# Optimization experiments

Hardware: AMD Instinct MI355X
Metric: run time of the kernel (lower is better)

## Reference

```python
import jax, jax.numpy as jnp
import numpy as np

B, N_O, N_Q = 2, 512, 512
POS_DIM, LATENT, HEADS, HEAD_DIM, OUT_DIM = 3, 256, 8, 32, 128
HD = HEADS * HEAD_DIM  # == LATENT here


def _lin(key, fan_in, fan_out):
    return jax.random.normal(key, (fan_in, fan_out), jnp.float32) / np.sqrt(fan_in)


def setup_inputs() -> dict:
    key = jax.random.key(0)
    ks = jax.random.split(key, 12)
    return {
        'h_obs': jax.random.normal(ks[0], (B, N_O, LATENT), jnp.float32),
        'pos_obs': jax.random.uniform(ks[1], (B, N_O, POS_DIM), jnp.float32),
        'pos_query': jax.random.uniform(ks[2], (B, N_Q, POS_DIM), jnp.float32),
        'fw1': _lin(ks[3], LATENT, LATENT), 'fb1': jnp.zeros((LATENT,), jnp.float32),
        'fw2': _lin(ks[4], LATENT, HD), 'fb2': jnp.zeros((HD,), jnp.float32),
        'log_sigma': jnp.zeros((HEADS,), jnp.float32),
        'kw1': _lin(ks[5], POS_DIM * 3, LATENT), 'kb1': jnp.zeros((LATENT,), jnp.float32),
        'kw2': _lin(ks[6], LATENT, HEADS), 'kb2': jnp.zeros((HEADS,), jnp.float32),
        'ow': _lin(ks[7], HD, OUT_DIM), 'ob': jnp.zeros((OUT_DIM,), jnp.float32),
        'vw': _lin(ks[8], HD, OUT_DIM), 'vb': jnp.zeros((OUT_DIM,), jnp.float32),
    }


def reference(h_obs, pos_obs, pos_query, fw1, fb1, fw2, fb2, log_sigma,
              kw1, kb1, kw2, kb2, ow, ob, vw, vb):
    Bv, No, _ = h_obs.shape
    Nq = pos_query.shape[1]
    # feature net -> values [B, H, N_o, D]
    v = jax.nn.relu(h_obs @ fw1 + fb1) @ fw2 + fb2
    v = v.reshape(Bv, No, HEADS, HEAD_DIM).transpose(0, 2, 1, 3)
    # pairwise relative positions [B, Nq, No, P]
    pos_q = pos_query[:, :, None, :]
    pos_o = pos_obs[:, None, :, :]
    rel = pos_q - pos_o
    dist2 = jnp.sum(rel ** 2, axis=-1)  # [B, Nq, No]
    sigma = jnp.exp(log_sigma)[None, :, None, None]
    rbf = jnp.exp(-dist2[:, None] / (sigma ** 2 + 1e-6))  # [B, H, Nq, No]
    # kernel MLP on concatenated pairwise positions [B, Nq, No, 3P] -> [B, H, Nq, No]
    ki = jnp.concatenate([
        jnp.broadcast_to(pos_q, (Bv, Nq, No, POS_DIM)),
        jnp.broadcast_to(pos_o, (Bv, Nq, No, POS_DIM)),
        rel], axis=-1)
    delta = (jax.nn.relu(ki @ kw1 + kb1) @ kw2 + kb2).transpose(0, 3, 1, 2)
    logits = jnp.log(rbf + 1e-8) + delta
    weights = jax.nn.softmax(logits, axis=-1)  # [B, H, Nq, No]
    # weighted mean over observations
    v_mean = jnp.einsum('bhqo,bhod->bhqd', weights, v)  # [B, H, Nq, D]
    h_query = v_mean.transpose(0, 2, 1, 3).reshape(Bv, Nq, HD)
    # weighted variance: sum_o w * (v_o - v_mean)^2
    residual = v[:, :, None, :, :] - v_mean[:, :, :, None, :]  # [B, H, Nq, No, D]
    var = jnp.sum(weights[..., None] * residual ** 2, axis=3)  # [B, H, Nq, D]
    var = var.transpose(0, 2, 1, 3).reshape(Bv, Nq, HD)
    mean = h_query @ ow + ob
    var_out = jax.nn.softplus(var @ vw + vb)
    return (mean, var_out)
```

## Files before the change

### kernel.cpp

```cpp
#include <hip/hip_runtime.h>
#include <math.h>

#define NB 2
#define NO 512
#define NQ 512
#define OUT_DIM 128
#define LPAD 516

typedef __attribute__((ext_vector_type(8))) _Float16 half8;
typedef __attribute__((ext_vector_type(4))) _Float16 half4;
typedef __attribute__((ext_vector_type(4))) float f32x4;

__device__ __forceinline__ float softplus_f(float x) {
  return x > 0.0f ? x + log1pf(expf(-x)) : log1pf(expf(x));
}
__device__ __forceinline__ half8 splat8(_Float16 v) {
  return (half8){v, v, v, v, v, v, v, v};
}
__device__ __forceinline__ half8 fma8(half8 a, half8 b, half8 c) {
  return __builtin_elementwise_fma(a, b, c);
}
__device__ __forceinline__ half8 max8(half8 a, half8 b) {
  return __builtin_elementwise_max(a, b);
}
__device__ __forceinline__ void gll16(const void* g, void* l) {
  __builtin_amdgcn_global_load_lds(
      (const __attribute__((address_space(1))) unsigned int*)g,
      (__attribute__((address_space(3))) unsigned int*)l, 16, 0, 0);
}

__global__ __launch_bounds__(1024) void prep_kernel(
    const float* __restrict__ h_obs, const float* __restrict__ fw1,
    const float* __restrict__ fb1, const float* __restrict__ fw2,
    const float* __restrict__ fb2, _Float16* __restrict__ VT)
{
  __shared__ float s_red[4][4][256];
  __shared__ float s_hid[4][256];
  const int n  = threadIdx.x & 255;
  const int ks = threadIdx.x >> 8;
  const int r0 = blockIdx.x * 4;
  const int k0 = ks * 64;
  float a0 = 0.f, a1 = 0.f, a2 = 0.f, a3 = 0.f;
  #pragma unroll 8
  for (int kk = 0; kk < 64; ++kk) {
    int k = k0 + kk;
    float w = fw1[k * 256 + n];
    a0 = fmaf(h_obs[(r0 + 0) * 256 + k], w, a0);
    a1 = fmaf(h_obs[(r0 + 1) * 256 + k], w, a1);
    a2 = fmaf(h_obs[(r0 + 2) * 256 + k], w, a2);
    a3 = fmaf(h_obs[(r0 + 3) * 256 + k], w, a3);
  }
  s_red[ks][0][n] = a0; s_red[ks][1][n] = a1;
  s_red[ks][2][n] = a2; s_red[ks][3][n] = a3;
  __syncthreads();
  if (ks == 0) {
    float bb = fb1[n];
    #pragma unroll
    for (int r = 0; r < 4; ++r) {
      float v = s_red[0][r][n] + s_red[1][r][n] + s_red[2][r][n] + s_red[3][r][n] + bb;
      s_hid[r][n] = fmaxf(v, 0.f);
    }
  }
  __syncthreads();
  float c0 = 0.f, c1 = 0.f, c2 = 0.f, c3 = 0.f;
  #pragma unroll 8
  for (int kk = 0; kk < 64; ++kk) {
    int k = k0 + kk;
    float w = fw2[k * 256 + n];
    c0 = fmaf(s_hid[0][k], w, c0);
    c1 = fmaf(s_hid[1][k], w, c1);
    c2 = fmaf(s_hid[2][k], w, c2);
    c3 = fmaf(s_hid[3][k], w, c3);
  }
  __syncthreads();
  s_red[ks][0][n] = c0; s_red[ks][1][n] = c1;
  s_red[ks][2][n] = c2; s_red[ks][3][n] = c3;
  __syncthreads();
  if (ks == 0) {
    float bb = fb2[n];
    float vr[4];
    #pragma unroll
    for (int r = 0; r < 4; ++r)
      vr[r] = s_red[0][r][n] + s_red[1][r][n] + s_red[2][r][n] + s_red[3][r][n] + bb;
    const int h  = n >> 5, d = n & 31;
    const int bb_ = r0 >> 9, o0 = r0 & 511;
    half4 pv;
    #pragma unroll
    for (int r = 0; r < 4; ++r) pv[r] = (_Float16)vr[r];
    *(half4*)(VT + ((size_t)((bb_ * 8 + h) * 32 + d)) * 512 + o0) = pv;
  }
}

__global__ __launch_bounds__(512, 4) void attn_fused(
    const _Float16* __restrict__ VT,
    const float* __restrict__ kw1,
    const float* __restrict__ kb1,
    const float* __restrict__ kw2,
    const float* __restrict__ kb2,
    const float* __restrict__ log_sigma,
    const float* __restrict__ pos_obs,
    const float* __restrict__ pos_query,
    float* __restrict__ HVg)
{
  __shared__ __align__(16) float s_logits[2][8 * LPAD];
  __shared__ __align__(16) _Float16 s_P16[2][8][520];
  __shared__ half8 s_Bh[512];
  __shared__ __align__(16) float s_pool[256];
  __shared__ __align__(16) float s_po[3][516];
  __shared__ __align__(16) _Float16 s_co[3][264];

  _Float16* s_aq2 = (_Float16*)s_pool;

  const int t   = threadIdx.x;
  const int bq0 = blockIdx.x * 2;
  const int b   = bq0 >> 9;

  float pqx[2], pqy[2], pqz[2];
  #pragma unroll
  for (int q = 0; q < 2; ++q) {
    pqx[q] = pos_query[(bq0 + q) * 3 + 0];
    pqy[q] = pos_query[(bq0 + q) * 3 + 1];
    pqz[q] = pos_query[(bq0 + q) * 3 + 2];
  }
  {
    const int q = t >> 8, j = t & 255;
    float c0 = kw1[0 * 256 + j] + kw1[6 * 256 + j];
    float c1 = kw1[1 * 256 + j] + kw1[7 * 256 + j];
    float c2 = kw1[2 * 256 + j] + kw1[8 * 256 + j];
    s_aq2[q * 256 + j] = (_Float16)
        fmaf(pqx[q], c0, fmaf(pqy[q], c1, fmaf(pqz[q], c2, kb1[j])));
  }
  if (t < 256) {
    const int j = t;
    s_co[0][j] = (_Float16)(kw1[3 * 256 + j] - kw1[6 * 256 + j]);
    s_co[1][j] = (_Float16)(kw1[4 * 256 + j] - kw1[7 * 256 + j]);
    s_co[2][j] = (_Float16)(kw1[5 * 256 + j] - kw1[8 * 256 + j]);
  }
  {
    const int o = t;
    const float* p = pos_obs + (size_t)(b * NO + o) * 3;
    float px = p[0], py = p[1], pz = p[2];
    s_po[0][o] = px; s_po[1][o] = py; s_po[2][o] = pz;
    float d2q[2];
    #pragma unroll
    for (int q = 0; q < 2; ++q) {
      float r0 = pqx[q] - px, r1 = pqy[q] - py, r2 = pqz[q] - pz;
      d2q[q] = r0 * r0 + r1 * r1 + r2 * r2;
    }
    #pragma unroll
    for (int h = 0; h < 8; ++h) {
      float sg  = __expf(log_sigma[h]);
      float inv = 1.0f / (sg * sg + 1e-6f);
      float kbv = kb2[h];
      s_logits[0][h * LPAD + o] = fmaxf(-d2q[0] * inv, -18.420681f) + kbv;
      s_logits[1][h * LPAD + o] = fmaxf(-d2q[1] * inv, -18.420681f) + kbv;
    }
  }
  {
    const int kstep = t >> 6, lane = t & 63;
    const int nh = lane & 15;
    const int kb_ = kstep * 32 + ((lane >> 4) & 3) * 8;
    half8 b8;
    #pragma unroll
    for (int i = 0; i < 8; ++i) {
      float v = (nh < 8) ? kw2[(kb_ + i) * 8 + nh] : 0.f;
      b8[i] = (_Float16)v;
    }
    s_Bh[kstep * 64 + lane] = b8;
  }
  __syncthreads();

  {
    const int wave = t >> 6, lane = t & 63;
    const int quad = lane >> 4, mrow = lane & 15;
    const int tb   = wave * 4;
    _Float16 pxh[4], pyh[4], pzh[4];
    #pragma unroll
    for (int jt = 0; jt < 4; ++jt) {
      const int o = (tb + jt) * 16 + mrow;
      pxh[jt] = (_Float16)s_po[0][o];
      pyh[jt] = (_Float16)s_po[1][o];
      pzh[jt] = (_Float16)s_po[2][o];
    }
    f32x4 C[2][4];
    #pragma unroll
    for (int q = 0; q < 2; ++q)
      #pragma unroll
      for (int jt = 0; jt < 4; ++jt) C[q][jt] = (f32x4){0.f, 0.f, 0.f, 0.f};

    const half8 z8 = {0, 0, 0, 0, 0, 0, 0, 0};
    #pragma unroll
    for (int kstep = 0; kstep < 8; ++kstep) {
      const int koff = kstep * 32 + quad * 8;
      half8 c0 = *(const half8*)&s_co[0][koff];
      half8 c1 = *(const half8*)&s_co[1][koff];
      half8 c2 = *(const half8*)&s_co[2][koff];
      half8 aq0 = *(const half8*)(s_aq2 + koff);
      half8 aq1 = *(const half8*)(s_aq2 + 256 + koff);
      half8 bh  = s_Bh[kstep * 64 + lane];
      #pragma unroll
      for (int jt = 0; jt < 4; ++jt) {
        half8 ao = fma8(splat8(pxh[jt]), c0,
                   fma8(splat8(pyh[jt]), c1, splat8(pzh[jt]) * c2));
        half8 a0 = max8(aq0 + ao, z8);
        half8 a1 = max8(aq1 + ao, z8);
        C[0][jt] = __builtin_amdgcn_mfma_f32_16x16x32_f16(a0, bh, C[0][jt], 0, 0, 0);
        C[1][jt] = __builtin_amdgcn_mfma_f32_16x16x32_f16(a1, bh, C[1][jt], 0, 0, 0);
      }
    }
    const int hh = lane & 15;
    if (hh < 8) {
      #pragma unroll
      for (int q = 0; q < 2; ++q)
        #pragma unroll
        for (int jt = 0; jt < 4; ++jt) {
          const int ob2 = (tb + jt) * 16 + quad * 4;
          #pragma unroll
          for (int r = 0; r < 4; ++r)
            s_logits[q][hh * LPAD + ob2 + r] += C[q][jt][r];
        }
    }
  }
  __syncthreads();

  {
    const int h = t >> 6, lane = t & 63;
    const int kg = lane >> 4, dl = lane & 15;
    char* stg0 = (char*)s_Bh + h * 1024;
    char* b1   = (char*)&s_logits[0][h * LPAD];
    char* b3   = b1 + 1024;
    char* b2   = (char*)&s_logits[1][h * LPAD];
    const _Float16* vsrc = VT + ((size_t)(b * 8 + h) << 14)
                         + (lane >> 1) * 512 + (lane & 1) * 8;
    gll16(vsrc, stg0);

    float invq0, invq1;
    {
      const float* pl0 = &s_logits[0][h * LPAD];
      const float* pl1 = &s_logits[1][h * LPAD];
      float l0[8], l1[8];
      float m0 = -1e30f, m1 = -1e30f;
      #pragma unroll
      for (int k = 0; k < 8; ++k) {
        l0[k] = pl0[k * 64 + lane];
        l1[k] = pl1[k * 64 + lane];
        m0 = fmaxf(m0, l0[k]);
        m1 = fmaxf(m1, l1[k]);
      }
      #pragma unroll
      for (int off = 32; off >= 1; off >>= 1) {
        m0 = fmaxf(m0, __shfl_xor(m0, off, 64));
        m1 = fmaxf(m1, __shfl_xor(m1, off, 64));
      }
      float s0 = 0.f, s1 = 0.f;
      _Float16* pp0 = &s_P16[0][h][0];
      _Float16* pp1 = &s_P16[1][h][0];
      #pragma unroll
      for (int k = 0; k < 8; ++k) {
        float p0 = __expf(l0[k] - m0);
        float p1 = __expf(l1[k] - m1);
        s0 += p0; s1 += p1;
        pp0[k * 64 + lane] = (_Float16)p0;
        pp1[k * 64 + lane] = (_Float16)p1;
      }
      #pragma unroll
      for (int off = 32; off >= 1; off >>= 1) {
        s0 += __shfl_xor(s0, off, 64);
        s1 += __shfl_xor(s1, off, 64);
      }
      invq0 = 1.0f / s0; invq1 = 1.0f / s1;
    }
    gll16(vsrc + 16, b1);
    gll16(vsrc + 32, b2);
    gll16(vsrc + 48, b3);

    const char* pE = ((kg & 2) ? b1 : stg0) + dl * 32 + (kg & 1) * 16;
    const char* pO = ((kg & 2) ? b3 : b2)   + dl * 32 + (kg & 1) * 16;
    const _Float16* pB = &s_P16[lane & 1][h][0];
    f32x4 Cm0 = {0.f, 0.f, 0.f, 0.f}, Cm1 = Cm0, Cv0 = Cm0, Cv1 = Cm0;
    #pragma unroll
    for (int kp = 0; kp < 8; ++kp) {
      asm volatile("s_waitcnt vmcnt(2)" ::: "memory");
      {
        half8 am0 = *(const half8*)(pE);
        half8 am1 = *(const half8*)(pE + 512);
        half8 pb  = *(const half8*)(pB + (2 * kp) * 32 + kg * 8);
        half8 av0 = am0 * am0;
        half8 av1 = am1 * am1;
        __builtin_amdgcn_s_setprio(1);
        Cm0 = __builtin_amdgcn_mfma_f32_16x16x32_f16(am0, pb, Cm0, 0, 0, 0);
        Cm1 = __builtin_amdgcn_mfma_f32_16x16x32_f16(am1, pb, Cm1, 0, 0, 0);
        Cv0 = __builtin_amdgcn_mfma_f32_16x16x32_f16(av0, pb, Cv0, 0, 0, 0);
        Cv1 = __builtin_amdgcn_mfma_f32_16x16x32_f16(av1, pb, Cv1, 0, 0, 0);
        __builtin_amdgcn_s_setprio(0);
      }
      if (kp < 7) {
        asm volatile("s_waitcnt lgkmcnt(0)" ::: "memory");
        gll16(vsrc + (4 * kp + 4) * 16, stg0);
        gll16(vsrc + (4 * kp + 5) * 16, b1);
      }
      if (kp < 7) asm volatile("s_waitcnt vmcnt(2)" ::: "memory");
      else        asm volatile("s_waitcnt vmcnt(0)" ::: "memory");
      {
        half8 am0 = *(const half8*)(pO);
        half8 am1 = *(const half8*)(pO + 512);
        half8 pb  = *(const half8*)(pB + (2 * kp + 1) * 32 + kg * 8);
        half8 av0 = am0 * am0;
        half8 av1 = am1 * am1;
        __builtin_amdgcn_s_setprio(1);
        Cm0 = __builtin_amdgcn_mfma_f32_16x16x32_f16(am0, pb, Cm0, 0, 0, 0);
        Cm1 = __builtin_amdgcn_mfma_f32_16x16x32_f16(am1, pb, Cm1, 0, 0, 0);
        Cv0 = __builtin_amdgcn_mfma_f32_16x16x32_f16(av0, pb, Cv0, 0, 0, 0);
        Cv1 = __builtin_amdgcn_mfma_f32_16x16x32_f16(av1, pb, Cv1, 0, 0, 0);
        __builtin_amdgcn_s_setprio(0);
      }
      if (kp < 7) {
        asm volatile("s_waitcnt lgkmcnt(0)" ::: "memory");
        gll16(vsrc + (4 * kp + 6) * 16, b2);
        gll16(vsrc + (4 * kp + 7) * 16, b3);
      }
    }
    const int nq = lane & 15;
    if (nq < 2) {
      const float iv = nq ? invq1 : invq0;
      const int dbase = h * 32 + kg * 4;
      f32x4 m0, v0, m1, v1;
      #pragma unroll
      for (int r = 0; r < 4; ++r) {
        float a = Cm0[r] * iv;
        m0[r] = a; v0[r] = fmaxf(Cv0[r] * iv - a * a, 0.f);
        float c = Cm1[r] * iv;
        m1[r] = c; v1[r] = fmaxf(Cv1[r] * iv - c * c, 0.f);
      }
      float* hvq = HVg + (size_t)(bq0 + nq) * 2 * 256;
      *(f32x4*)(hvq + 0 * 256 + dbase)      = m0;
      *(f32x4*)(hvq + 1 * 256 + dbase)      = v0;
      *(f32x4*)(hvq + 0 * 256 + dbase + 16) = m1;
      *(f32x4*)(hvq + 1 * 256 + dbase + 16) = v1;
    }
  }
}

__global__ __launch_bounds__(256) void proj_kernel(
    const float* __restrict__ HV,
    const float* __restrict__ ow, const float* __restrict__ obias,
    const float* __restrict__ vw, const float* __restrict__ vbias,
    float* __restrict__ out)
{
  const int t = threadIdx.x;
  const int mode = t >> 7, n = t & 127;
  const int q0 = blockIdx.x * 8;
  const float* W = mode ? vw : ow;
  float acc[8] = {0.f, 0.f, 0.f, 0.f, 0.f, 0.f, 0.f, 0.f};
  for (int k = 0; k < 256; k += 4) {
    float w0 = W[(k + 0) * 128 + n];
    float w1 = W[(k + 1) * 128 + n];
    float w2 = W[(k + 2) * 128 + n];
    float w3 = W[(k + 3) * 128 + n];
    #pragma unroll
    for (int qq = 0; qq < 8; ++qq) {
      float4 x = *(const float4*)&HV[((size_t)(q0 + qq) * 2 + mode) * 256 + k];
      acc[qq] = fmaf(x.w, w3, fmaf(x.z, w2, fmaf(x.y, w1, fmaf(x.x, w0, acc[qq]))));
    }
  }
  const float bias = mode ? vbias[n] : obias[n];
  #pragma unroll
  for (int qq = 0; qq < 8; ++qq) {
    float v = acc[qq] + bias;
    if (mode) v = softplus_f(v);
    out[(size_t)mode * (NB * NQ * OUT_DIM) + (size_t)(q0 + qq) * OUT_DIM + n] = v;
  }
}

extern "C" void kernel_launch(void* const* d_in, const int* in_sizes, int n_in,
                              void* d_out, int out_size, void* d_ws, size_t ws_size,
                              hipStream_t stream)
{
  const float* h_obs     = (const float*)d_in[0];
  const float* pos_obs   = (const float*)d_in[1];
  const float* pos_query = (const float*)d_in[2];
  const float* fw1       = (const float*)d_in[3];
  const float* fb1       = (const float*)d_in[4];
  const float* fw2       = (const float*)d_in[5];
  const float* fb2       = (const float*)d_in[6];
  const float* log_sigma = (const float*)d_in[7];
  const float* kw1       = (const float*)d_in[8];
  const float* kb1       = (const float*)d_in[9];
  const float* kw2       = (const float*)d_in[10];
  const float* kb2       = (const float*)d_in[11];
  const float* ow        = (const float*)d_in[12];
  const float* ob        = (const float*)d_in[13];
  const float* vw        = (const float*)d_in[14];
  const float* vb        = (const float*)d_in[15];

  float* out = (float*)d_out;
  _Float16* ws = (_Float16*)d_ws;
  _Float16* VT = ws;
  float*    HV = (float*)(ws + 262144);

  prep_kernel<<<256, 1024, 0, stream>>>(h_obs, fw1, fb1, fw2, fb2, VT);
  attn_fused<<<NB * NQ / 2, 512, 0, stream>>>(VT, kw1, kb1, kw2, kb2,
                                              log_sigma, pos_obs, pos_query, HV);
  proj_kernel<<<NB * NQ / 8, 256, 0, stream>>>(HV, ow, ob, vw, vb, out);
}
```

Before: 143.4 us.

## Repartition output projection: split-K across threads, fewer queries per block, more blocks

The output projection kernel now launches one block per (query pair, mode) instead of one block per 8 queries covering both modes. Within a block the 256-wide reduction is split into two halves across thread groups and combined through shared memory. This raises the block count from 128 to 1024 so more compute units are occupied, at the cost of re-reading weight rows more often and adding a shared-memory reduction plus barrier.

```diff
diff --git a/kernel.cpp b/kernel.cpp
--- a/kernel.cpp
+++ b/kernel.cpp
@@ -347,28 +347,40 @@
     const float* __restrict__ vw, const float* __restrict__ vbias,
     float* __restrict__ out)
 {
-  const int t = threadIdx.x;
-  const int mode = t >> 7, n = t & 127;
-  const int q0 = blockIdx.x * 8;
-  const float* W = mode ? vw : ow;
-  float acc[8] = {0.f, 0.f, 0.f, 0.f, 0.f, 0.f, 0.f, 0.f};
-  for (int k = 0; k < 256; k += 4) {
+  __shared__ float s_red[2][2][128];
+  const int t  = threadIdx.x;
+  const int n  = t & 127, ks = t >> 7;
+  const int mode = blockIdx.x & 1;
+  const int q0 = (blockIdx.x >> 1) * 2;
+  const float* W  = mode ? vw : ow;
+  const float* X0 = HV + ((size_t)(q0 + 0) * 2 + mode) * 256;
+  const float* X1 = HV + ((size_t)(q0 + 1) * 2 + mode) * 256;
+  float a0 = 0.f, a1 = 0.f;
+  const int k0 = ks * 128;
+  #pragma unroll 8
+  for (int k = k0; k < k0 + 128; k += 4) {
     float w0 = W[(k + 0) * 128 + n];
     float w1 = W[(k + 1) * 128 + n];
     float w2 = W[(k + 2) * 128 + n];
     float w3 = W[(k + 3) * 128 + n];
-    #pragma unroll
-    for (int qq = 0; qq < 8; ++qq) {
-      float4 x = *(const float4*)&HV[((size_t)(q0 + qq) * 2 + mode) * 256 + k];
-      acc[qq] = fmaf(x.w, w3, fmaf(x.z, w2, fmaf(x.y, w1, fmaf(x.x, w0, acc[qq]))));
-    }
-  }
-  const float bias = mode ? vbias[n] : obias[n];
-  #pragma unroll
-  for (int qq = 0; qq < 8; ++qq) {
-    float v = acc[qq] + bias;
-    if (mode) v = softplus_f(v);
-    out[(size_t)mode * (NB * NQ * OUT_DIM) + (size_t)(q0 + qq) * OUT_DIM + n] = v;
+    float4 x0 = *(const float4*)&X0[k];
+    float4 x1 = *(const float4*)&X1[k];
+    a0 = fmaf(x0.x, w0, a0); a1 = fmaf(x1.x, w0, a1);
+    a0 = fmaf(x0.y, w1, a0); a1 = fmaf(x1.y, w1, a1);
+    a0 = fmaf(x0.z, w2, a0); a1 = fmaf(x1.z, w2, a1);
+    a0 = fmaf(x0.w, w3, a0); a1 = fmaf(x1.w, w3, a1);
+  }
+  s_red[ks][0][n] = a0;
+  s_red[ks][1][n] = a1;
+  __syncthreads();
+  if (ks == 0) {
+    const float bias = mode ? vbias[n] : obias[n];
+    #pragma unroll
+    for (int qq = 0; qq < 2; ++qq) {
+      float v = s_red[0][qq][n] + s_red[1][qq][n] + bias;
+      if (mode) v = softplus_f(v);
+      out[(size_t)mode * (NB * NQ * OUT_DIM) + (size_t)(q0 + qq) * OUT_DIM + n] = v;
+    }
   }
 }
 
@@ -401,5 +413,5 @@
   prep_kernel<<<256, 1024, 0, stream>>>(h_obs, fw1, fb1, fw2, fb2, VT);
   attn_fused<<<NB * NQ / 2, 512, 0, stream>>>(VT, kw1, kb1, kw2, kb2,
                                               log_sigma, pos_obs, pos_query, HV);
-  proj_kernel<<<NB * NQ / 8, 256, 0, stream>>>(HV, ow, ob, vw, vb, out);
-}
+  proj_kernel<<<NB * NQ, 256, 0, stream>>>(HV, ow, ob, vw, vb, out);
+}
```

Result: faster. 134.6 us (-6.1%).

## Fuse output projection into attention kernel using fp16 packed weights

Applied to the files above, without the earlier changes.

Removes the separate projection kernel. The attention kernel now writes its per-query mean/variance to shared memory and applies the ow/vw projections plus bias and softplus in place. The prep kernel gets extra blocks that convert ow and vw into one fp16 [256x256] weight matrix. This saves a launch and the HV round trip through global memory. In exchange each attention block re-reads the full weight matrix, and the weights lose precision from the fp16 cast.

```diff
diff --git a/kernel.cpp b/kernel.cpp
--- a/kernel.cpp
+++ b/kernel.cpp
@@ -32,8 +32,20 @@
 __global__ __launch_bounds__(1024) void prep_kernel(
     const float* __restrict__ h_obs, const float* __restrict__ fw1,
     const float* __restrict__ fb1, const float* __restrict__ fw2,
-    const float* __restrict__ fb2, _Float16* __restrict__ VT)
+    const float* __restrict__ fb2,
+    const float* __restrict__ ow, const float* __restrict__ vw,
+    _Float16* __restrict__ VT, _Float16* __restrict__ W2h)
 {
+  if (blockIdx.x >= 256) {
+    const int i  = blockIdx.x - 256;
+    const int e0 = (i * 1024 + threadIdx.x) * 2;
+    const int k = e0 >> 8, col = e0 & 255;
+    float v0 = (col < 128) ? ow[k * 128 + col] : vw[k * 128 + col - 128];
+    float v1 = (col + 1 < 128) ? ow[k * 128 + col + 1] : vw[k * 128 + col - 127];
+    W2h[e0]     = (_Float16)v0;
+    W2h[e0 + 1] = (_Float16)v1;
+    return;
+  }
   __shared__ float s_red[4][4][256];
   __shared__ float s_hid[4][256];
   const int n  = threadIdx.x & 255;
@@ -93,6 +105,7 @@
 
 __global__ __launch_bounds__(512, 4) void attn_fused(
     const _Float16* __restrict__ VT,
+    const _Float16* __restrict__ W2h,
     const float* __restrict__ kw1,
     const float* __restrict__ kb1,
     const float* __restrict__ kw2,
@@ -100,7 +113,8 @@
     const float* __restrict__ log_sigma,
     const float* __restrict__ pos_obs,
     const float* __restrict__ pos_query,
-    float* __restrict__ HVg)
+    const float* __restrict__ obias, const float* __restrict__ vbias,
+    float* __restrict__ out)
 {
   __shared__ __align__(16) float s_logits[2][8 * LPAD];
   __shared__ __align__(16) _Float16 s_P16[2][8][520];
@@ -110,6 +124,7 @@
   __shared__ __align__(16) _Float16 s_co[3][264];
 
   _Float16* s_aq2 = (_Float16*)s_pool;
+  float*    s_hvx = (float*)s_po;
 
   const int t   = threadIdx.x;
   const int bq0 = blockIdx.x * 2;
@@ -332,43 +347,36 @@
         float c = Cm1[r] * iv;
         m1[r] = c; v1[r] = fmaxf(Cv1[r] * iv - c * c, 0.f);
       }
-      float* hvq = HVg + (size_t)(bq0 + nq) * 2 * 256;
-      *(f32x4*)(hvq + 0 * 256 + dbase)      = m0;
-      *(f32x4*)(hvq + 1 * 256 + dbase)      = v0;
-      *(f32x4*)(hvq + 0 * 256 + dbase + 16) = m1;
-      *(f32x4*)(hvq + 1 * 256 + dbase + 16) = v1;
-    }
-  }
-}
-
-__global__ __launch_bounds__(256) void proj_kernel(
-    const float* __restrict__ HV,
-    const float* __restrict__ ow, const float* __restrict__ obias,
-    const float* __restrict__ vw, const float* __restrict__ vbias,
-    float* __restrict__ out)
-{
-  const int t = threadIdx.x;
-  const int mode = t >> 7, n = t & 127;
-  const int q0 = blockIdx.x * 8;
-  const float* W = mode ? vw : ow;
-  float acc[8] = {0.f, 0.f, 0.f, 0.f, 0.f, 0.f, 0.f, 0.f};
-  for (int k = 0; k < 256; k += 4) {
-    float w0 = W[(k + 0) * 128 + n];
-    float w1 = W[(k + 1) * 128 + n];
-    float w2 = W[(k + 2) * 128 + n];
-    float w3 = W[(k + 3) * 128 + n];
-    #pragma unroll
-    for (int qq = 0; qq < 8; ++qq) {
-      float4 x = *(const float4*)&HV[((size_t)(q0 + qq) * 2 + mode) * 256 + k];
-      acc[qq] = fmaf(x.w, w3, fmaf(x.z, w2, fmaf(x.y, w1, fmaf(x.x, w0, acc[qq]))));
-    }
-  }
-  const float bias = mode ? vbias[n] : obias[n];
-  #pragma unroll
-  for (int qq = 0; qq < 8; ++qq) {
-    float v = acc[qq] + bias;
-    if (mode) v = softplus_f(v);
-    out[(size_t)mode * (NB * NQ * OUT_DIM) + (size_t)(q0 + qq) * OUT_DIM + n] = v;
+      *(f32x4*)(s_hvx + (nq * 2 + 0) * 256 + dbase)      = m0;
+      *(f32x4*)(s_hvx + (nq * 2 + 1) * 256 + dbase)      = v0;
+      *(f32x4*)(s_hvx + (nq * 2 + 0) * 256 + dbase + 16) = m1;
+      *(f32x4*)(s_hvx + (nq * 2 + 1) * 256 + dbase + 16) = v1;
+    }
+  }
+  __syncthreads();
+
+  {
+    const int row = t >> 7, n = t & 127;
+    const int m = row & 1, qq = row >> 1;
+    const float* X = s_hvx + row * 256;
+    const _Float16* Wp = W2h + (m * 128 + n);
+    float acc = 0.f;
+    #pragma unroll 4
+    for (int k0 = 0; k0 < 256; k0 += 8) {
+      float4 xa = *(const float4*)&X[k0];
+      float4 xb = *(const float4*)&X[k0 + 4];
+      acc = fmaf(xa.x, (float)Wp[(k0 + 0) * 256], acc);
+      acc = fmaf(xa.y, (float)Wp[(k0 + 1) * 256], acc);
+      acc = fmaf(xa.z, (float)Wp[(k0 + 2) * 256], acc);
+      acc = fmaf(xa.w, (float)Wp[(k0 + 3) * 256], acc);
+      acc = fmaf(xb.x, (float)Wp[(k0 + 4) * 256], acc);
+      acc = fmaf(xb.y, (float)Wp[(k0 + 5) * 256], acc);
+      acc = fmaf(xb.z, (float)Wp[(k0 + 6) * 256], acc);
+      acc = fmaf(xb.w, (float)Wp[(k0 + 7) * 256], acc);
+    }
+    float v = acc + (m ? vbias[n] : obias[n]);
+    if (m) v = softplus_f(v);
+    out[(size_t)m * (NB * NQ * OUT_DIM) + (size_t)(bq0 + qq) * OUT_DIM + n] = v;
   }
 }
 
@@ -395,11 +403,12 @@
 
   float* out = (float*)d_out;
   _Float16* ws = (_Float16*)d_ws;
-  _Float16* VT = ws;
-  float*    HV = (float*)(ws + 262144);
-
-  prep_kernel<<<256, 1024, 0, stream>>>(h_obs, fw1, fb1, fw2, fb2, VT);
-  attn_fused<<<NB * NQ / 2, 512, 0, stream>>>(VT, kw1, kb1, kw2, kb2,
-                                              log_sigma, pos_obs, pos_query, HV);
-  proj_kernel<<<NB * NQ / 8, 256, 0, stream>>>(HV, ow, ob, vw, vb, out);
-}
+  _Float16* VT  = ws;
+  _Float16* W2h = ws + 262144;
+
+  prep_kernel<<<288, 1024, 0, stream>>>(h_obs, fw1, fb1, fw2, fb2, ow, vw,
+                                        VT, W2h);
+  attn_fused<<<NB * NQ / 2, 512, 0, stream>>>(VT, W2h, kw1, kb1, kw2, kb2,
+                                              log_sigma, pos_obs, pos_query,
+                                              ob, vb, out);
+}
```

Result: faster. 130.4 us (-9.1%).
